# Kernel optimization log

Hardware: AMD Instinct MI355X
Metric: run time of the kernel (lower is better)

Reference implementation:

```python
import jax, jax.numpy as jnp
import numpy as np


def setup_inputs() -> dict:
    key = jax.random.key(0)
    k1, k2, k3 = jax.random.split(key, 3)
    L, B, T, H = 2, 16, 512, 12
    NUM_CUT = 1            # cuts per feature -> D+1 = 2 bins
    NUM_LEAF = (NUM_CUT + 1) ** H  # 4096
    NUM_CLASSES = 1000
    x = jax.random.normal(k1, (L, B, T, H), dtype=jnp.float32)
    cuts = jax.random.uniform(k2, (H, NUM_CUT), dtype=jnp.float32)
    leaf_score = jax.random.uniform(k3, (NUM_LEAF, NUM_CLASSES), dtype=jnp.float32)
    return {"x": x, "cuts": cuts, "leaf_score": leaf_score}


def reference(x, cuts, leaf_score):
    # Faithful to source: torch_bin RETURNS h (pre-softmax logits); temperature unused.
    xl = x[-1]                      # [B, T, H] -- only the last layer is used
    B, T, H = xl.shape
    D = cuts.shape[1]
    W = jnp.linspace(1.0, D + 1.0, D + 1).astype(xl.dtype)          # [D+1]
    sorted_cuts = jnp.sort(cuts, axis=-1)                            # [H, D]
    b = jnp.cumsum(
        jnp.concatenate([jnp.zeros((H, 1), dtype=xl.dtype), -sorted_cuts], axis=1),
        axis=1,
    )                                                                # [H, D+1]
    # h[b,t,f,:] = x[b,t,f] * W + b[f]  (outer product per scalar feature)
    h = xl[..., None] * W + b                                        # [B, T, H, D+1]
    # kron-product reduce over features -> leaf weights [B, T, (D+1)^H]
    leaf = h[..., 0, :]
    for i in range(1, H):
        leaf = (leaf[..., :, None] * h[..., i, None, :]).reshape(B, T, -1)
    out = jnp.einsum('btl,lc->btc', leaf, leaf_score)                # [B, T, C]
    return jnp.mean(out, axis=1)                                     # [B, C]
```

## Files before the change

### kernel.cpp

```cpp
#include <hip/hip_runtime.h>

#define HF 12
#define NLEAF 4096
#define NB 16
#define NT 512
#define NC 1000
#define NTC 8
#define TCH 64
#define TSUB 16
#define NSUB (TCH / TSUB)
#define LCH 64
#define NLCH (NLEAF / LCH)
#define NCT 4
#define INVT (1.0f / 512.0f)

__global__ __launch_bounds__(256) void k1_leaf(const float* __restrict__ x,
                                               const float* __restrict__ cuts,
                                               float* __restrict__ Sp) {
  const int blk = blockIdx.x;
  const int tid = threadIdx.x;

  __shared__ float h0s[TSUB][HF], h1s[TSUB][HF];
  __shared__ float Phis[TSUB][64], Plos[TSUB][64];

  const float* xb = x + (size_t)NB * NT * HF + (size_t)blk * (TCH * HF);

  const int  tl  = tid / HF;
  const int  f   = tid - tl * HF;
  const bool ldr = (tid < TSUB * HF);
  const float cf = ldr ? cuts[f] : 0.f;
  float xv = ldr ? xb[tid] : 0.f;

  float acc[16];
#pragma unroll
  for (int k = 0; k < 16; ++k) acc[k] = 0.f;

  const int w  = tid >> 6;
  const int lo = tid & 63;

  for (int ts = 0; ts < NSUB; ++ts) {
    if (ldr) {
      h0s[tl][f] = xv;
      h1s[tl][f] = 2.f * xv - cf;
    }
    __syncthreads();
    if (ldr && ts + 1 < NSUB) xv = xb[(ts + 1) * TSUB * HF + tid];

#pragma unroll
    for (int r = 0; r < 8; ++r) {
      const int task = r * 256 + tid;
      const int t2   = task >> 7;
      const int half = (task >> 6) & 1;
      const int idx  = task & 63;
      const float* hh0 = h0s[t2];
      const float* hh1 = h1s[t2];
      float p = 1.f;
#pragma unroll
      for (int i = 0; i < 6; ++i) {
        const int ff  = half * 6 + i;
        const int bit = (idx >> (5 - i)) & 1;
        p *= bit ? hh1[ff] : hh0[ff];
      }
      if (half) Plos[t2][idx] = p;
      else      Phis[t2][(idx & 3) * 16 + (idx >> 2)] = p;
    }
    __syncthreads();

#pragma unroll
    for (int t2 = 0; t2 < TSUB; ++t2) {
      const float  plo = Plos[t2][lo];
      const float4* ph = (const float4*)&Phis[t2][w * 16];
      const float4 p0 = ph[0], p1 = ph[1], p2 = ph[2], p3 = ph[3];
      acc[0]  += p0.x * plo;  acc[1]  += p0.y * plo;
      acc[2]  += p0.z * plo;  acc[3]  += p0.w * plo;
      acc[4]  += p1.x * plo;  acc[5]  += p1.y * plo;
      acc[6]  += p1.z * plo;  acc[7]  += p1.w * plo;
      acc[8]  += p2.x * plo;  acc[9]  += p2.y * plo;
      acc[10] += p2.z * plo;  acc[11] += p2.w * plo;
      acc[12] += p3.x * plo;  acc[13] += p3.y * plo;
      acc[14] += p3.z * plo;  acc[15] += p3.w * plo;
    }
  }

  float* sp = Sp + (size_t)blk * NLEAF;
#pragma unroll
  for (int k = 0; k < 16; ++k) sp[k * 256 + tid] = acc[k];
}

__global__ __launch_bounds__(256) void k15_sum(const float* __restrict__ Sp,
                                               float* __restrict__ St) {
  const int l = blockIdx.x * 256 + threadIdx.x;
  float s[NB];
#pragma unroll
  for (int b = 0; b < NB; ++b) {
    float v = 0.f;
#pragma unroll
    for (int tc = 0; tc < NTC; ++tc)
      v += Sp[(size_t)(b * NTC + tc) * NLEAF + l];
    s[b] = v * INVT;
  }
  float4* o = (float4*)&St[(size_t)l * NB];
  o[0] = make_float4(s[0],  s[1],  s[2],  s[3]);
  o[1] = make_float4(s[4],  s[5],  s[6],  s[7]);
  o[2] = make_float4(s[8],  s[9],  s[10], s[11]);
  o[3] = make_float4(s[12], s[13], s[14], s[15]);
}

__global__ __launch_bounds__(256) void k2_gemm(const float* __restrict__ St,
                                               const float* __restrict__ score,
                                               float* __restrict__ pout) {
  const int ct = blockIdx.x / NLCH;
  const int lc = blockIdx.x % NLCH;
  const int c  = ct * 256 + threadIdx.x;
  if (c >= NC) return;

  float acc[NB];
#pragma unroll
  for (int b = 0; b < NB; ++b) acc[b] = 0.f;

#pragma unroll 4
  for (int l = 0; l < LCH; ++l) {
    const int gl = lc * LCH + l;
    const float sv = score[(size_t)gl * NC + c];
    const float4* sr = (const float4*)&St[(size_t)gl * NB];
    const float4 a0 = sr[0], a1 = sr[1], a2 = sr[2], a3 = sr[3];
    acc[0]  += a0.x * sv;  acc[1]  += a0.y * sv;
    acc[2]  += a0.z * sv;  acc[3]  += a0.w * sv;
    acc[4]  += a1.x * sv;  acc[5]  += a1.y * sv;
    acc[6]  += a1.z * sv;  acc[7]  += a1.w * sv;
    acc[8]  += a2.x * sv;  acc[9]  += a2.y * sv;
    acc[10] += a2.z * sv;  acc[11] += a2.w * sv;
    acc[12] += a3.x * sv;  acc[13] += a3.y * sv;
    acc[14] += a3.z * sv;  acc[15] += a3.w * sv;
  }

  float4* po = (float4*)&pout[((size_t)lc * NC + c) * NB];
  po[0] = make_float4(acc[0],  acc[1],  acc[2],  acc[3]);
  po[1] = make_float4(acc[4],  acc[5],  acc[6],  acc[7]);
  po[2] = make_float4(acc[8],  acc[9],  acc[10], acc[11]);
  po[3] = make_float4(acc[12], acc[13], acc[14], acc[15]);
}

__global__ __launch_bounds__(256) void k3_red(const float* __restrict__ pout,
                                              float* __restrict__ out) {
  const int gid = blockIdx.x * 256 + threadIdx.x;
  if (gid >= NB * NC) return;
  const int b = gid / NC;
  const int c = gid - b * NC;
  float v = 0.f;
#pragma unroll 8
  for (int lc = 0; lc < NLCH; ++lc)
    v += pout[((size_t)lc * NC + c) * NB + b];
  out[gid] = v;
}

extern "C" void kernel_launch(void* const* d_in, const int* in_sizes, int n_in,
                              void* d_out, int out_size, void* d_ws, size_t ws_size,
                              hipStream_t stream) {
  const float* x     = (const float*)d_in[0];
  const float* cuts  = (const float*)d_in[1];
  const float* score = (const float*)d_in[2];
  float* out = (float*)d_out;

  float* Sp = (float*)d_ws;
  float* St = Sp + (size_t)NB * NTC * NLEAF;
  float* po = St + (size_t)NLEAF * NB;

  k1_leaf<<<NB * NTC, 256, 0, stream>>>(x, cuts, Sp);
  k15_sum<<<NLEAF / 256, 256, 0, stream>>>(Sp, St);
  k2_gemm<<<NCT * NLCH, 256, 0, stream>>>(St, score, po);
  k3_red<<<(NB * NC + 255) / 256, 256, 0, stream>>>(po, out);
}
```

Measured before the change: 95.83 us.

## Fuse time-chunk reduction into GEMM kernel via shared-memory leaf tile

Removes the separate k15_sum kernel. Each GEMM block now sums the per-time-chunk partial leaf sums for its 64-leaf slice into shared memory, then runs the score GEMM from that tile. The partial-output layout also changes to [lc][b][c], so both the GEMM stores and the k3 reduction loads are coalesced across classes. This saves a launch and the round trip through the St buffer, at the cost of each of the 4 class-tile blocks redundantly re-reducing the same Sp slice.

```diff
diff --git a/kernel.cpp b/kernel.cpp
--- a/kernel.cpp
+++ b/kernel.cpp
@@ -87,58 +87,49 @@
   for (int k = 0; k < 16; ++k) sp[k * 256 + tid] = acc[k];
 }
 
-__global__ __launch_bounds__(256) void k15_sum(const float* __restrict__ Sp,
-                                               float* __restrict__ St) {
-  const int l = blockIdx.x * 256 + threadIdx.x;
-  float s[NB];
-#pragma unroll
-  for (int b = 0; b < NB; ++b) {
+__global__ __launch_bounds__(256) void k2f(const float* __restrict__ Sp,
+                                           const float* __restrict__ score,
+                                           float* __restrict__ pout) {
+  const int lc  = blockIdx.x / NCT;
+  const int ct  = blockIdx.x % NCT;
+  const int tid = threadIdx.x;
+
+  __shared__ float Stl[NB][LCH];
+
+  for (int i = tid; i < NB * LCH; i += 256) {
+    const int b  = i >> 6;
+    const int ll = i & 63;
+    const float* sp = Sp + (size_t)(b * NTC) * NLEAF + lc * LCH + ll;
     float v = 0.f;
 #pragma unroll
-    for (int tc = 0; tc < NTC; ++tc)
-      v += Sp[(size_t)(b * NTC + tc) * NLEAF + l];
-    s[b] = v * INVT;
+    for (int tc = 0; tc < NTC; ++tc) v += sp[(size_t)tc * NLEAF];
+    Stl[b][ll] = v * INVT;
   }
-  float4* o = (float4*)&St[(size_t)l * NB];
-  o[0] = make_float4(s[0],  s[1],  s[2],  s[3]);
-  o[1] = make_float4(s[4],  s[5],  s[6],  s[7]);
-  o[2] = make_float4(s[8],  s[9],  s[10], s[11]);
-  o[3] = make_float4(s[12], s[13], s[14], s[15]);
-}
+  __syncthreads();
 
-__global__ __launch_bounds__(256) void k2_gemm(const float* __restrict__ St,
-                                               const float* __restrict__ score,
-                                               float* __restrict__ pout) {
-  const int ct = blockIdx.x / NLCH;
-  const int lc = blockIdx.x % NLCH;
-  const int c  = ct * 256 + threadIdx.x;
-  if (c >= NC) return;
+  const int c = ct * 256 + tid;
+  if (c < NC) {
+    float acc[NB];
+#pragma unroll
+    for (int b = 0; b < NB; ++b) acc[b] = 0.f;
 
-  float acc[NB];
+    const float* sc = score + (size_t)(lc * LCH) * NC + c;
+    for (int l0 = 0; l0 < LCH; l0 += 8) {
+      float sv[8];
 #pragma unroll
-  for (int b = 0; b < NB; ++b) acc[b] = 0.f;
-
-#pragma unroll 4
-  for (int l = 0; l < LCH; ++l) {
-    const int gl = lc * LCH + l;
-    const float sv = score[(size_t)gl * NC + c];
-    const float4* sr = (const float4*)&St[(size_t)gl * NB];
-    const float4 a0 = sr[0], a1 = sr[1], a2 = sr[2], a3 = sr[3];
-    acc[0]  += a0.x * sv;  acc[1]  += a0.y * sv;
-    acc[2]  += a0.z * sv;  acc[3]  += a0.w * sv;
-    acc[4]  += a1.x * sv;  acc[5]  += a1.y * sv;
-    acc[6]  += a1.z * sv;  acc[7]  += a1.w * sv;
-    acc[8]  += a2.x * sv;  acc[9]  += a2.y * sv;
-    acc[10] += a2.z * sv;  acc[11] += a2.w * sv;
-    acc[12] += a3.x * sv;  acc[13] += a3.y * sv;
-    acc[14] += a3.z * sv;  acc[15] += a3.w * sv;
+      for (int j = 0; j < 8; ++j) sv[j] = sc[(size_t)(l0 + j) * NC];
+#pragma unroll
+      for (int b = 0; b < NB; ++b) {
+        const float4* r = (const float4*)&Stl[b][l0];
+        const float4 r0 = r[0], r1 = r[1];
+        acc[b] += r0.x * sv[0] + r0.y * sv[1] + r0.z * sv[2] + r0.w * sv[3]
+                + r1.x * sv[4] + r1.y * sv[5] + r1.z * sv[6] + r1.w * sv[7];
+      }
+    }
+#pragma unroll
+    for (int b = 0; b < NB; ++b)
+      pout[((size_t)lc * NB + b) * NC + c] = acc[b];
   }
-
-  float4* po = (float4*)&pout[((size_t)lc * NC + c) * NB];
-  po[0] = make_float4(acc[0],  acc[1],  acc[2],  acc[3]);
-  po[1] = make_float4(acc[4],  acc[5],  acc[6],  acc[7]);
-  po[2] = make_float4(acc[8],  acc[9],  acc[10], acc[11]);
-  po[3] = make_float4(acc[12], acc[13], acc[14], acc[15]);
 }
 
 __global__ __launch_bounds__(256) void k3_red(const float* __restrict__ pout,
@@ -150,7 +141,7 @@
   float v = 0.f;
 #pragma unroll 8
   for (int lc = 0; lc < NLCH; ++lc)
-    v += pout[((size_t)lc * NC + c) * NB + b];
+    v += pout[((size_t)lc * NB + b) * NC + c];
   out[gid] = v;
 }
 
@@ -163,11 +154,9 @@
   float* out = (float*)d_out;
 
   float* Sp = (float*)d_ws;
-  float* St = Sp + (size_t)NB * NTC * NLEAF;
-  float* po = St + (size_t)NLEAF * NB;
+  float* po = Sp + (size_t)NB * NTC * NLEAF;
 
   k1_leaf<<<NB * NTC, 256, 0, stream>>>(x, cuts, Sp);
-  k15_sum<<<NLEAF / 256, 256, 0, stream>>>(Sp, St);
-  k2_gemm<<<NCT * NLCH, 256, 0, stream>>>(St, score, po);
+  k2f<<<NLCH * NCT, 256, 0, stream>>>(Sp, score, po);
   k3_red<<<(NB * NC + 255) / 256, 256, 0, stream>>>(po, out);
 }
```

New measurement: 88.12 us. -8.0%, faster.
